# Performance work log

Measured on AMD Instinct MI355X. Metric: run time of the kernel, lower is better.

The kernel has to match this reference:

```python
import jax, jax.numpy as jnp
import numpy as np

N = 100000      # nodes
E = 800000      # edges (avg degree 8)
F = 5           # num_node_features
D = 128         # embed_dim
H = 4           # heads
HD = D // H     # per-head dim = 32
H1, H2 = 64, 128  # mlp hidden dims


def _mlp(x, W1, b1, W2, b2, W3, b3):
    h = jax.nn.relu(x @ W1 + b1)
    h = jax.nn.relu(h @ W2 + b2)
    return h @ W3 + b3


def setup_inputs() -> dict:
    key = jax.random.key(0)
    ks = jax.random.split(key, 24)
    g = lambda i, shape: (jax.random.normal(ks[i], shape, dtype=jnp.float32) * 0.05)
    z = lambda d: jnp.zeros((d,), dtype=jnp.float32)
    return {
        "x": jax.random.normal(ks[0], (N, F), dtype=jnp.float32),
        "edge_index": jax.random.randint(ks[1], (2, E), 0, N),
        # mlp_prep: F -> 64 -> 128 -> D
        "prep_W1": g(2, (F, H1)),  "prep_b1": z(H1),
        "prep_W2": g(3, (H1, H2)), "prep_b2": z(H2),
        "prep_W3": g(4, (H2, D)),  "prep_b3": z(D),
        # mlp_update: D -> 64 -> 128 -> D
        "upd_W1": g(5, (D, H1)),   "upd_b1": z(H1),
        "upd_W2": g(6, (H1, H2)),  "upd_b2": z(H2),
        "upd_W3": g(7, (H2, D)),   "upd_b3": z(D),
        # TransformerConv projections (heads=4, per-head 32, concat -> D)
        "q_W": g(8, (D, D)),  "q_b": z(D),
        "k_W": g(9, (D, D)),  "k_b": z(D),
        "v_W": g(10, (D, D)), "v_b": z(D),
        "skip_W": g(11, (D, D)), "skip_b": z(D),
    }


def _transformer_conv(x, edge_index, q_W, q_b, k_W, k_b, v_W, v_b, skip_W, skip_b):
    # PyG TransformerConv: messages flow src=edge_index[0] -> dst=edge_index[1]
    src, dst = edge_index[0], edge_index[1]
    q = (x @ q_W + q_b).reshape(N, H, HD)
    k = (x @ k_W + k_b).reshape(N, H, HD)
    v = (x @ v_W + v_b).reshape(N, H, HD)
    scale = 1.0 / np.sqrt(HD).astype(np.float32)
    # per-edge attention logits [E, H]
    score = jnp.einsum('ehd,ehd->eh', q[dst], k[src]) * scale
    # segment softmax over incoming edges of each destination node
    m = jax.ops.segment_max(score, dst, num_segments=N)          # [N, H]
    e = jnp.exp(score - m[dst])                                  # [E, H]
    denom = jax.ops.segment_sum(e, dst, num_segments=N)         # [N, H]
    alpha = e / denom[dst]                                       # [E, H]
    # scatter-aggregate weighted values
    agg = jax.ops.segment_sum(alpha[..., None] * v[src], dst, num_segments=N)  # [N, H, HD]
    return agg.reshape(N, H * HD) + (x @ skip_W + skip_b)


def reference(x, edge_index,
              prep_W1, prep_b1, prep_W2, prep_b2, prep_W3, prep_b3,
              upd_W1, upd_b1, upd_W2, upd_b2, upd_W3, upd_b3,
              q_W, q_b, k_W, k_b, v_W, v_b, skip_W, skip_b):
    h_init = _mlp(x, prep_W1, prep_b1, prep_W2, prep_b2, prep_W3, prep_b3)
    h = _transformer_conv(h_init, edge_index, q_W, q_b, k_W, k_b, v_W, v_b, skip_W, skip_b)
    return h + _mlp(h, upd_W1, upd_b1, upd_W2, upd_b2, upd_W3, upd_b3)
```

## Files before the change

kernel.cpp:

```cpp
#include <hip/hip_runtime.h>
#include <hip/hip_bf16.h>

#define N_  100000
#define F_  5
#define D_  128
#define H_  4
#define HD_ 32
#define E_  800000

typedef __attribute__((ext_vector_type(8))) short bf16x8;
typedef __attribute__((ext_vector_type(4))) float f32x4;

__device__ __forceinline__ unsigned short f2bf(float f) {
  unsigned u = __float_as_uint(f);
  u += 0x7FFF + ((u >> 16) & 1);
  return (unsigned short)(u >> 16);
}

__device__ __forceinline__ unsigned pk2(float a, float b) {
  __hip_bfloat162 h = __float22bfloat162_rn(make_float2(a, b));
  return *(unsigned*)&h;
}

__device__ __forceinline__ float2 bf2f2(unsigned u) {
  float2 r;
  r.x = __uint_as_float(u << 16);
  r.y = __uint_as_float(u & 0xffff0000u);
  return r;
}

__device__ __forceinline__ float rowsum8(float x) {
  x += __int_as_float(__builtin_amdgcn_update_dpp(0, __float_as_int(x), 0x0B1, 0xF, 0xF, false));
  x += __int_as_float(__builtin_amdgcn_update_dpp(0, __float_as_int(x), 0x04E, 0xF, 0xF, false));
  x += __int_as_float(__builtin_amdgcn_update_dpp(0, __float_as_int(x), 0x141, 0xF, 0xF, false));
  return x;
}

template<int K, int M>
__device__ __forceinline__ void wconv_one(const float* __restrict__ W,
                                          unsigned short* __restrict__ WT,
                                          int idx) {
  const int r = idx & 7;
  const int l = (idx >> 3) & 15;
  const int rest = idx >> 7;
  const int kq = rest % (K / 8);
  const int i  = rest / (K / 8);
  WT[idx] = f2bf(W[(kq * 8 + r) * M + i * 16 + l]);
}

#define WCONV_NB 480
#define SCAN_NB ((N_ + 255) / 256)

__global__ __launch_bounds__(256) void k_wconv_all(
    const float* __restrict__ w0, const float* __restrict__ w1,
    const float* __restrict__ w2, const float* __restrict__ w3,
    const float* __restrict__ w4, const float* __restrict__ w5,
    const float* __restrict__ w6, const float* __restrict__ w7,
    const float* __restrict__ w8, unsigned short* __restrict__ WT,
    int* __restrict__ deg)
{
  if (blockIdx.x >= WCONV_NB) {
    const int i = (blockIdx.x - WCONV_NB) * 256 + threadIdx.x;
    if (i < N_) deg[i] = 0;
    return;
  }
  const int idx = blockIdx.x * 256 + threadIdx.x;
  if (idx < 8192)        wconv_one<64, 128>(w0, WT,          idx);
  else if (idx < 24576)  wconv_one<128,128>(w1, WT + 8192,   idx - 8192);
  else if (idx < 40960)  wconv_one<128,128>(w2, WT + 24576,  idx - 24576);
  else if (idx < 57344)  wconv_one<128,128>(w3, WT + 40960,  idx - 40960);
  else if (idx < 73728)  wconv_one<128,128>(w4, WT + 57344,  idx - 57344);
  else if (idx < 90112)  wconv_one<128,128>(w5, WT + 73728,  idx - 73728);
  else if (idx < 98304)  wconv_one<128, 64>(w6, WT + 90112,  idx - 90112);
  else if (idx < 106496) wconv_one<64, 128>(w7, WT + 98304,  idx - 98304);
  else                   wconv_one<128,128>(w8, WT + 106496, idx - 106496);
}

template<int K, int M>
__device__ __forceinline__ void gemm_frag(const unsigned short* sX,
                                          const unsigned short* __restrict__ WT,
                                          f32x4 (*acc)[4],
                                          int wr, int wc, int l16, int kg)
{
  constexpr int SX = K + 8;
  constexpr int IF = M / 32;
  #pragma unroll
  for (int i = 0; i < IF; ++i)
    #pragma unroll
    for (int j = 0; j < 4; ++j) acc[i][j] = (f32x4){0.f, 0.f, 0.f, 0.f};
  #pragma unroll
  for (int k0 = 0; k0 < K; k0 += 32) {
    const int kq = k0 / 8 + kg;
    bf16x8 aw[IF];
    #pragma unroll
    for (int i = 0; i < IF; ++i)
      aw[i] = *(const bf16x8*)&WT[(((wr * IF + i) * (K / 8) + kq) * 16 + l16) * 8];
    #pragma unroll
    for (int j = 0; j < 4; ++j) {
      const bf16x8 bx = *(const bf16x8*)&sX[(wc * 64 + j * 16 + l16) * SX + k0 + kg * 8];
      #pragma unroll
      for (int i = 0; i < IF; ++i)
        acc[i][j] = __builtin_amdgcn_mfma_f32_16x16x32_bf16(aw[i], bx, acc[i][j], 0, 0, 0);
    }
  }
}

template<int M, bool RELU, int SXO>
__device__ __forceinline__ void acc_to_lds(unsigned short* sY, f32x4 (*acc)[4],
                                           const float* __restrict__ bias,
                                           int wr, int wc, int l16, int kg)
{
  constexpr int IF = M / 32;
  float4 b4[IF];
  #pragma unroll
  for (int i = 0; i < IF; ++i)
    b4[i] = *(const float4*)&bias[(wr * IF + i) * 16 + kg * 4];
  #pragma unroll
  for (int j = 0; j < 4; ++j) {
    const int row = wc * 64 + j * 16 + l16;
    #pragma unroll
    for (int i = 0; i < IF; ++i) {
      const int f0 = (wr * IF + i) * 16 + kg * 4;
      float ox = acc[i][j][0] + b4[i].x, oy = acc[i][j][1] + b4[i].y;
      float oz = acc[i][j][2] + b4[i].z, ow = acc[i][j][3] + b4[i].w;
      if constexpr (RELU) {
        ox = fmaxf(ox, 0.f); oy = fmaxf(oy, 0.f);
        oz = fmaxf(oz, 0.f); ow = fmaxf(ow, 0.f);
      }
      uint2 p;
      p.x = pk2(ox, oy);
      p.y = pk2(oz, ow);
      *(uint2*)&sY[row * SXO + f0] = p;
    }
  }
}

__global__ __launch_bounds__(256) void k_prep_proj(
    const float* __restrict__ x,
    const float* __restrict__ pW1, const float* __restrict__ pb1,
    const unsigned short* __restrict__ wt_p2, const float* __restrict__ pb2,
    const unsigned short* __restrict__ wt_p3, const float* __restrict__ pb3,
    const unsigned short* __restrict__ wt_q, const float* __restrict__ qb,
    const unsigned short* __restrict__ wt_k, const float* __restrict__ kb,
    const unsigned short* __restrict__ wt_v, const float* __restrict__ vb,
    const unsigned short* __restrict__ wt_s, const float* __restrict__ sb,
    unsigned short* __restrict__ q16, unsigned short* __restrict__ k16,
    unsigned short* __restrict__ v16, float* __restrict__ out)
{
  __shared__ __align__(16) unsigned short bufA[128 * 72];
  __shared__ __align__(16) unsigned short bufB[128 * 136];

  const int t = threadIdx.x;
  const int node0 = blockIdx.x * 128;
  const int lane = t & 63;
  const int w  = t >> 6;
  const int wr = w >> 1, wc = w & 1;
  const int l16 = lane & 15, kg = lane >> 4;

  float* sxs = (float*)bufB;
  float* sw1 = (float*)bufB + 640;
  {
    const long gbase = (long)node0 * F_;
    for (int i = t; i < 128 * F_; i += 256) {
      const long g = gbase + i;
      sxs[i] = (g < (long)N_ * F_) ? x[g] : 0.f;
    }
    for (int i = t; i < 384; i += 256)
      sw1[i] = (i < 320) ? pW1[i] : pb1[i - 320];
  }
  __syncthreads();

  {
    const int n = t >> 1;
    const int half = (t & 1) * 32;
    float xr[F_];
    #pragma unroll
    for (int k = 0; k < F_; ++k) xr[k] = sxs[n * F_ + k];
    const float* sb1 = sw1 + 320;
    #pragma unroll
    for (int q = 0; q < 8; ++q) {
      float o[4];
      #pragma unroll
      for (int jj = 0; jj < 4; ++jj) {
        const int f = half + q * 4 + jj;
        float a = sb1[f];
        #pragma unroll
        for (int k = 0; k < F_; ++k) a = fmaf(xr[k], sw1[k * 64 + f], a);
        o[jj] = fmaxf(a, 0.f);
      }
      uint2 pkd;
      pkd.x = pk2(o[0], o[1]);
      pkd.y = pk2(o[2], o[3]);
      *(uint2*)&bufA[n * 72 + half + q * 4] = pkd;
    }
  }
  __syncthreads();

  f32x4 acc[4][4];

  gemm_frag<64, 128>(bufA, wt_p2, acc, wr, wc, l16, kg);
  acc_to_lds<128, true, 136>(bufB, acc, pb2, wr, wc, l16, kg);
  __syncthreads();

  gemm_frag<128, 128>(bufB, wt_p3, acc, wr, wc, l16, kg);
  __syncthreads();
  acc_to_lds<128, false, 136>(bufB, acc, pb3, wr, wc, l16, kg);
  __syncthreads();

  {
    const unsigned short* wtsP[3] = {wt_q, wt_k, wt_v};
    const float* bsP[3] = {qb, kb, vb};
    unsigned short* ysP[3] = {q16, k16, v16};
    #pragma unroll
    for (int ws = 0; ws < 3; ++ws) {
      gemm_frag<128, 128>(bufB, wtsP[ws], acc, wr, wc, l16, kg);
      const float* __restrict__ bias = bsP[ws];
      unsigned short* __restrict__ Yb = ysP[ws];
      float4 b4[4];
      #pragma unroll
      for (int i = 0; i < 4; ++i)
        b4[i] = *(const float4*)&bias[(wr * 4 + i) * 16 + kg * 4];
      #pragma unroll
      for (int j = 0; j < 4; ++j) {
        const int node = node0 + wc * 64 + j * 16 + l16;
        if (node >= N_) continue;
        #pragma unroll
        for (int i = 0; i < 4; ++i) {
          const int f0 = (wr * 4 + i) * 16 + kg * 4;
          uint2 ob;
          ob.x = pk2(acc[i][j][0] + b4[i].x, acc[i][j][1] + b4[i].y);
          ob.y = pk2(acc[i][j][2] + b4[i].z, acc[i][j][3] + b4[i].w);
          *(uint2*)&Yb[(long)node * D_ + f0] = ob;
        }
      }
    }
  }

  gemm_frag<128, 128>(bufB, wt_s, acc, wr, wc, l16, kg);
  {
    float4 b4[4];
    #pragma unroll
    for (int i = 0; i < 4; ++i)
      b4[i] = *(const float4*)&sb[(wr * 4 + i) * 16 + kg * 4];
    #pragma unroll
    for (int j = 0; j < 4; ++j) {
      const int node = node0 + wc * 64 + j * 16 + l16;
      if (node >= N_) continue;
      #pragma unroll
      for (int i = 0; i < 4; ++i) {
        const int f0 = (wr * 4 + i) * 16 + kg * 4;
        float4 o = make_float4(acc[i][j][0] + b4[i].x, acc[i][j][1] + b4[i].y,
                               acc[i][j][2] + b4[i].z, acc[i][j][3] + b4[i].w);
        *(float4*)&out[(long)node * D_ + f0] = o;
      }
    }
  }
}

__global__ __launch_bounds__(256) void k_update(
    const unsigned short* __restrict__ wt_u1, const float* __restrict__ ub1,
    const unsigned short* __restrict__ wt_u2, const float* __restrict__ ub2,
    const unsigned short* __restrict__ wt_u3, const float* __restrict__ ub3,
    float* __restrict__ out)
{
  __shared__ __align__(16) unsigned short bufA[128 * 72];
  __shared__ __align__(16) unsigned short bufB[128 * 136];

  const int t = threadIdx.x;
  const int node0 = blockIdx.x * 128;
  const int lane = t & 63;
  const int w  = t >> 6;
  const int wr = w >> 1, wc = w & 1;
  const int l16 = lane & 15, kg = lane >> 4;

  #pragma unroll
  for (int i = 0; i < 16; ++i) {
    const int g = t + 256 * i;
    const int row = g >> 5;
    const int kc  = g & 31;
    const int node = node0 + row;
    float4 xv = (node < N_) ? ((const float4*)out)[(long)node * 32 + kc]
                            : make_float4(0.f, 0.f, 0.f, 0.f);
    uint2 p;
    p.x = pk2(xv.x, xv.y);
    p.y = pk2(xv.z, xv.w);
    *(uint2*)&bufB[row * 136 + kc * 4] = p;
  }
  __syncthreads();

  f32x4 acc[4][4];

  gemm_frag<128, 64>(bufB, wt_u1, acc, wr, wc, l16, kg);
  acc_to_lds<64, true, 72>(bufA, acc, ub1, wr, wc, l16, kg);
  __syncthreads();

  gemm_frag<64, 128>(bufA, wt_u2, acc, wr, wc, l16, kg);
  acc_to_lds<128, true, 136>(bufB, acc, ub2, wr, wc, l16, kg);
  __syncthreads();

  gemm_frag<128, 128>(bufB, wt_u3, acc, wr, wc, l16, kg);
  {
    float4 b4[4];
    #pragma unroll
    for (int i = 0; i < 4; ++i)
      b4[i] = *(const float4*)&ub3[(wr * 4 + i) * 16 + kg * 4];
    #pragma unroll
    for (int j = 0; j < 4; ++j) {
      const int node = node0 + wc * 64 + j * 16 + l16;
      if (node >= N_) continue;
      #pragma unroll
      for (int i = 0; i < 4; ++i) {
        const int f0 = (wr * 4 + i) * 16 + kg * 4;
        const float4 r = *(const float4*)&out[(long)node * D_ + f0];
        float4 o = make_float4(acc[i][j][0] + b4[i].x + r.x,
                               acc[i][j][1] + b4[i].y + r.y,
                               acc[i][j][2] + b4[i].z + r.z,
                               acc[i][j][3] + b4[i].w + r.w);
        *(float4*)&out[(long)node * D_ + f0] = o;
      }
    }
  }
}

__global__ __launch_bounds__(256) void k_hist(const int* __restrict__ ei,
                                              int* __restrict__ deg) {
  int e = blockIdx.x * 256 + threadIdx.x;
  if (e < E_) atomicAdd(&deg[ei[E_ + e]], 1);
}

__global__ __launch_bounds__(256) void k_scan1(const int* __restrict__ deg,
                                               int* __restrict__ off,
                                               int* __restrict__ bsum) {
  __shared__ int s[256];
  const int t = threadIdx.x;
  const int i = blockIdx.x * 256 + t;
  const int v = (i < N_) ? deg[i] : 0;
  s[t] = v;
  __syncthreads();
  #pragma unroll
  for (int o = 1; o < 256; o <<= 1) {
    int u = (t >= o) ? s[t - o] : 0;
    __syncthreads();
    s[t] += u;
    __syncthreads();
  }
  if (i < N_) off[i] = s[t] - v;
  if (t == 255) bsum[blockIdx.x] = s[255];
}

__global__ __launch_bounds__(256) void k_scan23(int* __restrict__ off,
                                                const int* __restrict__ bsum,
                                                int* __restrict__ cur) {
  __shared__ int sacc[256];
  const int t = threadIdx.x;
  const int bid = blockIdx.x;
  int s = 0;
  for (int j = t; j < bid; j += 256) s += bsum[j];
  sacc[t] = s;
  __syncthreads();
  #pragma unroll
  for (int o = 128; o > 0; o >>= 1) {
    if (t < o) sacc[t] += sacc[t + o];
    __syncthreads();
  }
  const int prefix = sacc[0];
  const int i = bid * 256 + t;
  if (i < N_) {
    const int o = off[i] + prefix;
    off[i] = o;
    cur[i] = o;
  }
}

__global__ __launch_bounds__(256) void k_fill(const int* __restrict__ ei,
                                              int* __restrict__ cur,
                                              int* __restrict__ esrc) {
  int e = blockIdx.x * 256 + threadIdx.x;
  if (e < E_) {
    int src = ei[e], dst = ei[E_ + e];
    int pos = atomicAdd(&cur[dst], 1);
    esrc[pos] = src;
  }
}

__global__ __launch_bounds__(256) void k_attn(
    const int* __restrict__ esrc, const int* __restrict__ off,
    const int* __restrict__ deg,
    const unsigned short* __restrict__ q,
    const unsigned short* __restrict__ kbuf,
    const unsigned short* __restrict__ vbuf,
    float* __restrict__ out)
{
  const int node = blockIdx.x * 4 + (threadIdx.x >> 6);
  const int lane = threadIdx.x & 63;
  if (node >= N_) return;

  const int start = off[node];
  const int cnt   = deg[node];
  const int end   = start + cnt;
  const int h = lane >> 5;
  const int c = lane & 31;
  const float C = 0.17677669529663687f * 1.4426950408889634f;

  const uint2 qu = *(const uint2*)&q[(long)node * D_ + 4 * c];
  const float2 q01 = bf2f2(qu.x), q23 = bf2f2(qu.y);
  const float qx0 = q01.x * C, qx1 = q01.y * C;
  const float qx2 = q23.x * C, qx3 = q23.y * C;

  float m = -__builtin_inff(), l = 0.f;
  float a0 = 0.f, a1 = 0.f, a2 = 0.f, a3 = 0.f;

  const int P = (cnt + 1) >> 1;
  if (P > 0) {
    int e = start + h;
    bool v_cur = e < end;
    int i_cur = esrc[v_cur ? e : start];
    const int e1 = e + 2;
    bool v_nxt = e1 < end;
    int i_nxt = esrc[v_nxt ? e1 : start];

    uint2 kc = *(const uint2*)&kbuf[(long)i_cur * D_ + 4 * c];
    uint2 vc = *(const uint2*)&vbuf[(long)i_cur * D_ + 4 * c];

    for (int p = 0; ; ++p) {
      const bool more = (p + 1) < P;
      uint2 kn, vn;
      int i_n2 = 0;
      bool v_n2 = false;
      if (more) {
        kn = *(const uint2*)&kbuf[(long)i_nxt * D_ + 4 * c];
        vn = *(const uint2*)&vbuf[(long)i_nxt * D_ + 4 * c];
        const int e2 = start + 2 * (p + 2) + h;
        v_n2 = e2 < end;
        i_n2 = esrc[v_n2 ? e2 : start];
      }

      const float2 k01 = bf2f2(kc.x), k23 = bf2f2(kc.y);
      float ps = fmaf(qx0, k01.x, fmaf(qx1, k01.y, fmaf(qx2, k23.x, qx3 * k23.y)));
      ps = rowsum8(ps);
      ps = v_cur ? ps : -__builtin_inff();

      const float mn = fmaxf(m, ps);
      const float s  = __builtin_amdgcn_exp2f(fmaxf(m  - mn, -200.f));
      const float ee = __builtin_amdgcn_exp2f(fmaxf(ps - mn, -200.f));
      const float2 v01 = bf2f2(vc.x), v23 = bf2f2(vc.y);
      l  = fmaf(l,  s, ee);
      a0 = fmaf(a0, s, ee * v01.x);
      a1 = fmaf(a1, s, ee * v01.y);
      a2 = fmaf(a2, s, ee * v23.x);
      a3 = fmaf(a3, s, ee * v23.y);
      m = mn;

      if (!more) break;
      v_cur = v_nxt; kc = kn; vc = vn;
      v_nxt = v_n2;  i_nxt = i_n2;
    }
  }

  const float mB = __shfl_xor(m, 32);
  const float lB = __shfl_xor(l, 32);
  const float b0 = __shfl_xor(a0, 32);
  const float b1 = __shfl_xor(a1, 32);
  const float b2 = __shfl_xor(a2, 32);
  const float b3 = __shfl_xor(a3, 32);

  const float mm = fmaxf(m, mB);
  const float sA = __builtin_amdgcn_exp2f(fmaxf(m  - mm, -200.f));
  const float sB = __builtin_amdgcn_exp2f(fmaxf(mB - mm, -200.f));
  const float L  = fmaf(l, sA, lB * sB);

  if (h == 0 && L > 0.f) {
    const float inv = 1.0f / L;
    float4* op = (float4*)&out[(long)node * D_ + 4 * c];
    float4 cv = *op;
    cv.x += fmaf(a0, sA, b0 * sB) * inv;
    cv.y += fmaf(a1, sA, b1 * sB) * inv;
    cv.z += fmaf(a2, sA, b2 * sB) * inv;
    cv.w += fmaf(a3, sA, b3 * sB) * inv;
    *op = cv;
  }
}

extern "C" void kernel_launch(void* const* d_in, const int* in_sizes, int n_in,
                              void* d_out, int out_size, void* d_ws, size_t ws_size,
                              hipStream_t stream) {
  const float* x   = (const float*)d_in[0];
  const int*   ei  = (const int*)d_in[1];
  const float* pW1 = (const float*)d_in[2];  const float* pb1 = (const float*)d_in[3];
  const float* pW2 = (const float*)d_in[4];  const float* pb2 = (const float*)d_in[5];
  const float* pW3 = (const float*)d_in[6];  const float* pb3 = (const float*)d_in[7];
  const float* uW1 = (const float*)d_in[8];  const float* ub1 = (const float*)d_in[9];
  const float* uW2 = (const float*)d_in[10]; const float* ub2 = (const float*)d_in[11];
  const float* uW3 = (const float*)d_in[12]; const float* ub3 = (const float*)d_in[13];
  const float* qW  = (const float*)d_in[14]; const float* qb  = (const float*)d_in[15];
  const float* kW  = (const float*)d_in[16]; const float* kb  = (const float*)d_in[17];
  const float* vW  = (const float*)d_in[18]; const float* vb  = (const float*)d_in[19];
  const float* sW  = (const float*)d_in[20]; const float* sb  = (const float*)d_in[21];

  float* out = (float*)d_out;
  float* ws  = (float*)d_ws;

  const long ND = (long)N_ * D_;
  unsigned short* q16 = (unsigned short*)(ws + ND);
  unsigned short* k16 = (unsigned short*)(ws + 2 * ND);
  unsigned short* v16 = (unsigned short*)(ws + 3 * ND);

  unsigned short* wtb = (unsigned short*)(ws + 4 * ND);
  unsigned short* wt_p2 = wtb;
  unsigned short* wt_p3 = wtb + 8192;
  unsigned short* wt_q  = wtb + 24576;
  unsigned short* wt_k  = wtb + 40960;
  unsigned short* wt_v  = wtb + 57344;
  unsigned short* wt_s  = wtb + 73728;
  unsigned short* wt_u1 = wtb + 90112;
  unsigned short* wt_u2 = wtb + 98304;
  unsigned short* wt_u3 = wtb + 106496;

  int* deg  = (int*)ws;
  int* off  = deg + N_;
  int* cur  = off + N_;
  int* esrc = cur + N_;
  int* bsum = esrc + E_;

  const int gT = (N_ + 127) / 128;

  k_wconv_all<<<WCONV_NB + SCAN_NB, 256, 0, stream>>>(
      pW2, pW3, qW, kW, vW, sW, uW1, uW2, uW3, wtb, deg);

  k_hist  <<<(E_ + 255) / 256, 256, 0, stream>>>(ei, deg);
  k_scan1 <<<SCAN_NB, 256, 0, stream>>>(deg, off, bsum);
  k_scan23<<<SCAN_NB, 256, 0, stream>>>(off, bsum, cur);
  k_fill  <<<(E_ + 255) / 256, 256, 0, stream>>>(ei, cur, esrc);

  k_prep_proj<<<gT, 256, 0, stream>>>(
      x, pW1, pb1, wt_p2, pb2, wt_p3, pb3,
      wt_q, qb, wt_k, kb, wt_v, vb, wt_s, sb,
      q16, k16, v16, out);

  k_attn<<<(N_ + 3) / 4, 256, 0, stream>>>(esrc, off, deg, q16, k16, v16, out);

  k_update<<<gT, 256, 0, stream>>>(wt_u1, ub1, wt_u2, ub2, wt_u3, ub3, out);
}
```

Before: 357.8 us.

## Drop running max in edge softmax and process two edges per half-wave

The attention kernel no longer keeps an online max. It accumulates exp2 of the scaled logits directly, which removes the per-edge rescale exps and the max merge across half-waves. Each half-wave now handles two edges per iteration, giving four edges in flight per node, with K, V and index prefetch one iteration ahead. Offset and degree are packed into one int2 array written by the scan kernel, and the kernel uses 32-bit index arithmetic. Without max subtraction, large logits could overflow exp2, so correctness depends on scores staying small.

```diff
diff --git a/kernel.cpp b/kernel.cpp
--- a/kernel.cpp
+++ b/kernel.cpp
@@ -348,9 +348,11 @@
   if (t == 255) bsum[blockIdx.x] = s[255];
 }
 
-__global__ __launch_bounds__(256) void k_scan23(int* __restrict__ off,
+__global__ __launch_bounds__(256) void k_scan23(const int* __restrict__ off,
                                                 const int* __restrict__ bsum,
-                                                int* __restrict__ cur) {
+                                                int* __restrict__ cur,
+                                                const int* __restrict__ deg,
+                                                int2* __restrict__ meta) {
   __shared__ int sacc[256];
   const int t = threadIdx.x;
   const int bid = blockIdx.x;
@@ -367,8 +369,8 @@
   const int i = bid * 256 + t;
   if (i < N_) {
     const int o = off[i] + prefix;
-    off[i] = o;
     cur[i] = o;
+    meta[i] = make_int2(o, deg[i]);
   }
 }
 
@@ -384,8 +386,7 @@
 }
 
 __global__ __launch_bounds__(256) void k_attn(
-    const int* __restrict__ esrc, const int* __restrict__ off,
-    const int* __restrict__ deg,
+    const int* __restrict__ esrc, const int2* __restrict__ meta,
     const unsigned short* __restrict__ q,
     const unsigned short* __restrict__ kbuf,
     const unsigned short* __restrict__ vbuf,
@@ -395,88 +396,91 @@
   const int lane = threadIdx.x & 63;
   if (node >= N_) return;
 
-  const int start = off[node];
-  const int cnt   = deg[node];
-  const int end   = start + cnt;
+  const int2 md = meta[node];
+  const int start = md.x, cnt = md.y;
+  const int end = start + cnt;
   const int h = lane >> 5;
   const int c = lane & 31;
   const float C = 0.17677669529663687f * 1.4426950408889634f;
 
-  const uint2 qu = *(const uint2*)&q[(long)node * D_ + 4 * c];
+  const uint2 qu = *(const uint2*)&q[((unsigned)node << 7) + 4u * c];
   const float2 q01 = bf2f2(qu.x), q23 = bf2f2(qu.y);
   const float qx0 = q01.x * C, qx1 = q01.y * C;
   const float qx2 = q23.x * C, qx3 = q23.y * C;
 
-  float m = -__builtin_inff(), l = 0.f;
-  float a0 = 0.f, a1 = 0.f, a2 = 0.f, a3 = 0.f;
-
-  const int P = (cnt + 1) >> 1;
+  float l = 0.f, a0 = 0.f, a1 = 0.f, a2 = 0.f, a3 = 0.f;
+
+  const int P = (cnt + 3) >> 2;
   if (P > 0) {
-    int e = start + h;
-    bool v_cur = e < end;
-    int i_cur = esrc[v_cur ? e : start];
-    const int e1 = e + 2;
-    bool v_nxt = e1 < end;
-    int i_nxt = esrc[v_nxt ? e1 : start];
-
-    uint2 kc = *(const uint2*)&kbuf[(long)i_cur * D_ + 4 * c];
-    uint2 vc = *(const uint2*)&vbuf[(long)i_cur * D_ + 4 * c];
-
-    for (int p = 0; ; ++p) {
-      const bool more = (p + 1) < P;
-      uint2 kn, vn;
-      int i_n2 = 0;
-      bool v_n2 = false;
+    int eA = start + 2 * h, eB = eA + 1;
+    bool vAc = eA < end, vBc = eB < end;
+    unsigned iA = esrc[vAc ? eA : start];
+    unsigned iB = esrc[vBc ? eB : start];
+    uint2 kA = *(const uint2*)&kbuf[(iA << 7) + 4u * c];
+    uint2 kB = *(const uint2*)&kbuf[(iB << 7) + 4u * c];
+    uint2 wA = *(const uint2*)&vbuf[(iA << 7) + 4u * c];
+    uint2 wB = *(const uint2*)&vbuf[(iB << 7) + 4u * c];
+    int eA1 = eA + 4, eB1 = eB + 4;
+    bool vA1 = eA1 < end, vB1 = eB1 < end;
+    unsigned iA1 = esrc[vA1 ? eA1 : start];
+    unsigned iB1 = esrc[vB1 ? eB1 : start];
+
+    for (int it = 0;;) {
+      const bool more = (it + 1) < P;
+      uint2 kAn, kBn, wAn, wBn;
+      unsigned iA2 = 0, iB2 = 0;
+      bool vA2 = false, vB2 = false;
       if (more) {
-        kn = *(const uint2*)&kbuf[(long)i_nxt * D_ + 4 * c];
-        vn = *(const uint2*)&vbuf[(long)i_nxt * D_ + 4 * c];
-        const int e2 = start + 2 * (p + 2) + h;
-        v_n2 = e2 < end;
-        i_n2 = esrc[v_n2 ? e2 : start];
+        kAn = *(const uint2*)&kbuf[(iA1 << 7) + 4u * c];
+        kBn = *(const uint2*)&kbuf[(iB1 << 7) + 4u * c];
+        wAn = *(const uint2*)&vbuf[(iA1 << 7) + 4u * c];
+        wBn = *(const uint2*)&vbuf[(iB1 << 7) + 4u * c];
+        const int eA2 = start + 4 * (it + 2) + 2 * h;
+        const int eB2 = eA2 + 1;
+        vA2 = eA2 < end; vB2 = eB2 < end;
+        iA2 = esrc[vA2 ? eA2 : start];
+        iB2 = esrc[vB2 ? eB2 : start];
       }
 
-      const float2 k01 = bf2f2(kc.x), k23 = bf2f2(kc.y);
-      float ps = fmaf(qx0, k01.x, fmaf(qx1, k01.y, fmaf(qx2, k23.x, qx3 * k23.y)));
-      ps = rowsum8(ps);
-      ps = v_cur ? ps : -__builtin_inff();
-
-      const float mn = fmaxf(m, ps);
-      const float s  = __builtin_amdgcn_exp2f(fmaxf(m  - mn, -200.f));
-      const float ee = __builtin_amdgcn_exp2f(fmaxf(ps - mn, -200.f));
-      const float2 v01 = bf2f2(vc.x), v23 = bf2f2(vc.y);
-      l  = fmaf(l,  s, ee);
-      a0 = fmaf(a0, s, ee * v01.x);
-      a1 = fmaf(a1, s, ee * v01.y);
-      a2 = fmaf(a2, s, ee * v23.x);
-      a3 = fmaf(a3, s, ee * v23.y);
-      m = mn;
+      const float2 ka01 = bf2f2(kA.x), ka23 = bf2f2(kA.y);
+      const float2 kb01 = bf2f2(kB.x), kb23 = bf2f2(kB.y);
+      float sA = fmaf(qx0, ka01.x, fmaf(qx1, ka01.y, fmaf(qx2, ka23.x, qx3 * ka23.y)));
+      float sB = fmaf(qx0, kb01.x, fmaf(qx1, kb01.y, fmaf(qx2, kb23.x, qx3 * kb23.y)));
+      sA = rowsum8(sA);
+      sB = rowsum8(sB);
+      const float eAe = vAc ? __builtin_amdgcn_exp2f(sA) : 0.f;
+      const float eBe = vBc ? __builtin_amdgcn_exp2f(sB) : 0.f;
+      const float2 va01 = bf2f2(wA.x), va23 = bf2f2(wA.y);
+      const float2 vb01 = bf2f2(wB.x), vb23 = bf2f2(wB.y);
+      l += eAe + eBe;
+      a0 = fmaf(eAe, va01.x, fmaf(eBe, vb01.x, a0));
+      a1 = fmaf(eAe, va01.y, fmaf(eBe, vb01.y, a1));
+      a2 = fmaf(eAe, va23.x, fmaf(eBe, vb23.x, a2));
+      a3 = fmaf(eAe, va23.y, fmaf(eBe, vb23.y, a3));
 
       if (!more) break;
-      v_cur = v_nxt; kc = kn; vc = vn;
-      v_nxt = v_n2;  i_nxt = i_n2;
-    }
-  }
-
-  const float mB = __shfl_xor(m, 32);
-  const float lB = __shfl_xor(l, 32);
-  const float b0 = __shfl_xor(a0, 32);
-  const float b1 = __shfl_xor(a1, 32);
-  const float b2 = __shfl_xor(a2, 32);
-  const float b3 = __shfl_xor(a3, 32);
-
-  const float mm = fmaxf(m, mB);
-  const float sA = __builtin_amdgcn_exp2f(fmaxf(m  - mm, -200.f));
-  const float sB = __builtin_amdgcn_exp2f(fmaxf(mB - mm, -200.f));
-  const float L  = fmaf(l, sA, lB * sB);
-
-  if (h == 0 && L > 0.f) {
-    const float inv = 1.0f / L;
-    float4* op = (float4*)&out[(long)node * D_ + 4 * c];
+      ++it;
+      kA = kAn; kB = kBn; wA = wAn; wB = wBn;
+      vAc = vA1; vBc = vB1;
+      vA1 = vA2; vB1 = vB2;
+      iA1 = iA2; iB1 = iB2;
+    }
+  }
+
+  l  += __shfl_xor(l, 32);
+  a0 += __shfl_xor(a0, 32);
+  a1 += __shfl_xor(a1, 32);
+  a2 += __shfl_xor(a2, 32);
+  a3 += __shfl_xor(a3, 32);
+
+  if (h == 0 && l > 0.f) {
+    const float inv = 1.0f / l;
+    float4* op = (float4*)&out[((unsigned)node << 7) + 4u * c];
     float4 cv = *op;
-    cv.x += fmaf(a0, sA, b0 * sB) * inv;
-    cv.y += fmaf(a1, sA, b1 * sB) * inv;
-    cv.z += fmaf(a2, sA, b2 * sB) * inv;
-    cv.w += fmaf(a3, sA, b3 * sB) * inv;
+    cv.x += a0 * inv;
+    cv.y += a1 * inv;
+    cv.z += a2 * inv;
+    cv.w += a3 * inv;
     *op = cv;
   }
 }
@@ -521,6 +525,7 @@
   int* cur  = off + N_;
   int* esrc = cur + N_;
   int* bsum = esrc + E_;
+  int2* meta = (int2*)(bsum + 512);
 
   const int gT = (N_ + 127) / 128;
 
@@ -529,7 +534,7 @@
 
   k_hist  <<<(E_ + 255) / 256, 256, 0, stream>>>(ei, deg);
   k_scan1 <<<SCAN_NB, 256, 0, stream>>>(deg, off, bsum);
-  k_scan23<<<SCAN_NB, 256, 0, stream>>>(off, bsum, cur);
+  k_scan23<<<SCAN_NB, 256, 0, stream>>>(off, bsum, cur, deg, meta);
   k_fill  <<<(E_ + 255) / 256, 256, 0, stream>>>(ei, cur, esrc);
 
   k_prep_proj<<<gT, 256, 0, stream>>>(
@@ -537,7 +542,7 @@
       wt_q, qb, wt_k, kb, wt_v, vb, wt_s, sb,
       q16, k16, v16, out);
 
-  k_attn<<<(N_ + 3) / 4, 256, 0, stream>>>(esrc, off, deg, q16, k16, v16, out);
+  k_attn<<<(N_ + 3) / 4, 256, 0, stream>>>(esrc, meta, q16, k16, v16, out);
 
   k_update<<<gT, 256, 0, stream>>>(wt_u1, ub1, wt_u2, ub2, wt_u3, ub3, out);
 }
```

After: 366.2 us. +2.3%, slower.
